# Performance work log

Measured on AMD Instinct MI355X. Metric: run time of the kernel, lower is better.

## Reference

```python
import jax, jax.numpy as jnp
import numpy as np

B, T, C, SIZE = 2, 4096, 1024, 1024
ROPE_DIM = 64
GAMMA = 0.96


def setup_inputs() -> dict:
    key = jax.random.key(0)
    ks = jax.random.split(key, 8)
    x = jax.random.normal(ks[0], (B, T, C), dtype=jnp.float32)
    group_mask = jax.random.randint(ks[1], (B, T), 0, 2).astype(jnp.float32)
    att_mask = jnp.ones((B, T), dtype=jnp.float32)
    # torch init: randn(in, out) / in
    W_Q = jax.random.normal(ks[2], (C, SIZE), dtype=jnp.float32) / C
    W_K = jax.random.normal(ks[3], (C, SIZE), dtype=jnp.float32) / C
    W_V = jax.random.normal(ks[4], (C, SIZE), dtype=jnp.float32) / C
    fc_w = jax.random.normal(ks[5], (SIZE, SIZE), dtype=jnp.float32) / np.float32(np.sqrt(SIZE))
    fc_b = jnp.zeros((SIZE,), dtype=jnp.float32)
    return dict(x=x, group_mask=group_mask, att_mask=att_mask,
                W_Q=W_Q, W_K=W_K, W_V=W_V, fc_w=fc_w, fc_b=fc_b)


def _rope(t, offset):
    # lucidrains rotate_queries_or_keys: rotate first ROPE_DIM features of
    # the last dim, interleaved-pair rotation, positions along axis -2.
    seq = t.shape[-2]
    inv = 1.0 / (10000.0 ** (jnp.arange(0, ROPE_DIM, 2, dtype=jnp.float32) / ROPE_DIM))
    pos = jnp.arange(seq, dtype=jnp.float32) + offset
    freqs = pos[:, None] * inv[None, :]              # [T, D/2]
    freqs = jnp.repeat(freqs, 2, axis=-1)            # [T, D]
    cos, sin = jnp.cos(freqs), jnp.sin(freqs)
    t_rot, t_pass = t[..., :ROPE_DIM], t[..., ROPE_DIM:]
    x1, x2 = t_rot[..., 0::2], t_rot[..., 1::2]
    rot_half = jnp.stack([-x2, x1], axis=-1).reshape(t_rot.shape)
    t_rot = t_rot * cos + rot_half * sin
    return jnp.concatenate([t_rot, t_pass], axis=-1)


def reference(x, group_mask, att_mask, W_Q, W_K, W_V, fc_w, fc_b):
    Bx, Tx, _ = x.shape
    # _qkv with apply_rope=True, apply_act=True (ReLU)
    Q = jax.nn.relu(_rope(x @ W_Q, 0))               # [B,T,SIZE]
    K = jax.nn.relu(_rope(x @ W_K, 0))
    V = jax.nn.relu(x @ W_V)
    n = jnp.arange(Tx)[:, None]
    m = jnp.arange(Tx)[None, :]
    causal = (n >= m)
    # decay mask D[n,m] = gamma^(n-m) for n>=m else 0
    D = jnp.where(causal, jnp.float32(GAMMA) ** (n - m).astype(jnp.float32), 0.0)
    # group mask G[b,n,m] = group_mask[b, n-m] for n>=m else 0
    idx = jnp.clip(n - m, 0, Tx - 1)                 # [T,T]
    G = group_mask[:, idx] * causal.astype(x.dtype)  # [B,T,T]
    A = jnp.einsum('bnd,bmd->bnm', Q, K)
    A = A * att_mask[:, :, None]                     # attention mask
    A = A * D[None, :, :]                            # decay mask
    A = A * G                                        # group mask
    y = jnp.einsum('bnm,bmd->bnd', A, V)
    y = y @ fc_w + fc_b
    return y
```

## Files before the change

### kernel.cpp

```cpp
#include <hip/hip_runtime.h>
#include <stdint.h>

typedef __attribute__((ext_vector_type(4))) float f32x4;
typedef __attribute__((ext_vector_type(8))) __bf16 bf16x8;
typedef __attribute__((ext_vector_type(4))) unsigned short u16x4;
typedef __attribute__((ext_vector_type(8))) unsigned short u16x8;

#define DEV __device__ __forceinline__

DEV unsigned short f2bf(float f) {
  union { float f; unsigned int u; } v; v.f = f;
  unsigned int r = v.u + 0x7fffu + ((v.u >> 16) & 1u);
  return (unsigned short)(r >> 16);
}

DEV void gl_lds16(const void* g, void* l) {
  __builtin_amdgcn_global_load_lds(
      (const __attribute__((address_space(1))) unsigned int*)g,
      (__attribute__((address_space(3))) unsigned int*)l, 16, 0, 0);
}


__global__ void prep_tabs(const float* __restrict__ gm,
                          float* __restrict__ costab, float* __restrict__ sintab,
                          float* __restrict__ wtab) {
  int idx = blockIdx.x * 256 + threadIdx.x;
  int n = idx >> 6, c = idx & 63, j = c >> 1;
  float inv = powf(10000.0f, -(float)(2 * j) / 64.0f);
  float ang = (float)n * inv;
  costab[idx] = cosf(ang);
  sintab[idx] = sinf(ang);
  if (idx < 1024) {
    int b = idx >> 9, d = idx & 511;
    wtab[idx] = gm[b * 4096 + d] * powf(0.96f, (float)d);
  }
}

__global__ void cvt_x(const float* __restrict__ x, unsigned short* __restrict__ xb) {
  size_t i8 = ((size_t)blockIdx.x * 256 + threadIdx.x) * 8;
  float4 a = *(const float4*)(x + i8);
  float4 b = *(const float4*)(x + i8 + 4);
  u16x8 o;
  o[0] = f2bf(a.x); o[1] = f2bf(a.y); o[2] = f2bf(a.z); o[3] = f2bf(a.w);
  o[4] = f2bf(b.x); o[5] = f2bf(b.y); o[6] = f2bf(b.z); o[7] = f2bf(b.w);
  *(u16x8*)(xb + i8) = o;
}

__global__ void transpose_cvt4(const float* __restrict__ s0, const float* __restrict__ s1,
                               const float* __restrict__ s2, const float* __restrict__ s3,
                               unsigned short* __restrict__ d0, unsigned short* __restrict__ d3) {
  __shared__ float tile[32][33];
  int z = blockIdx.z;
  const float* src = (z == 0) ? s0 : (z == 1) ? s1 : (z == 2) ? s2 : s3;
  unsigned short* dst = (z == 3) ? d3 : d0 + (size_t)z * 1024 * 1024;
  int tx = threadIdx.x & 31, ty = threadIdx.x >> 5;
  int c0 = blockIdx.x * 32, r0 = blockIdx.y * 32;
  #pragma unroll
  for (int j = 0; j < 4; j++)
    tile[ty + 8 * j][tx] = src[(size_t)(r0 + ty + 8 * j) * 1024 + c0 + tx];
  __syncthreads();
  #pragma unroll
  for (int j = 0; j < 4; j++)
    dst[(size_t)(c0 + ty + 8 * j) * 1024 + r0 + tx] = f2bf(tile[tx][ty + 8 * j]);
}

template<int EPI>
__global__ void __launch_bounds__(256, 4)
gemm128(const unsigned short* __restrict__ A,
        const unsigned short* __restrict__ Bt,
        unsigned short* __restrict__ q_out,
        unsigned short* __restrict__ k_out,
        unsigned short* __restrict__ vt_out,
        const float* __restrict__ costab,
        const float* __restrict__ sintab,
        float* __restrict__ f_out,
        const float* __restrict__ bias)
{
  constexpr int K = 1024;
  __shared__ char smem[32768];
  char* a_sm = smem;
  char* b_sm = smem + 16384;
  const int tid = threadIdx.x;
  const int lane = tid & 63;
  const int w = tid >> 6;
  const int wm = w >> 1, wn = w & 1;
  const int bm = blockIdx.x, bn = blockIdx.y;

  const f32x4 fz = {0.f, 0.f, 0.f, 0.f};
  f32x4 acc[4][4];
  #pragma unroll
  for (int i = 0; i < 4; i++)
    #pragma unroll
    for (int j = 0; j < 4; j++) acc[i][j] = fz;

  const unsigned short* Abase = A + (size_t)bm * 128 * K;
  const unsigned short* Bbase = Bt + (size_t)bn * 128 * K;

  for (int k0 = 0; k0 < K; k0 += 64) {
    __syncthreads();
    #pragma unroll
    for (int i = 0; i < 4; i++) {
      int tg = i * 256 + tid;
      int row = tg >> 3;
      int sl = (tg & 7) ^ (row & 7);
      gl_lds16(Abase + (size_t)row * K + k0 + sl * 8, a_sm + tg * 16);
    }
    #pragma unroll
    for (int i = 0; i < 4; i++) {
      int tg = i * 256 + tid;
      int row = tg >> 3;
      int sl = (tg & 7) ^ (row & 7);
      gl_lds16(Bbase + (size_t)row * K + k0 + sl * 8, b_sm + tg * 16);
    }
    __syncthreads();
    #pragma unroll
    for (int ks = 0; ks < 2; ks++) {
      int kb = ks * 64 + ((lane >> 4) << 4);
      bf16x8 af[4], bfv[4];
      #pragma unroll
      for (int f = 0; f < 4; f++) {
        int ar = wm * 64 + f * 16 + (lane & 15);
        af[f] = *(const bf16x8*)(a_sm + ar * 128 + (kb ^ ((ar & 7) << 4)));
        int br = wn * 64 + f * 16 + (lane & 15);
        bfv[f] = *(const bf16x8*)(b_sm + br * 128 + (kb ^ ((br & 7) << 4)));
      }
      #pragma unroll
      for (int fm = 0; fm < 4; fm++)
        #pragma unroll
        for (int fn = 0; fn < 4; fn++)
          acc[fm][fn] = __builtin_amdgcn_mfma_f32_16x16x32_bf16(af[fm], bfv[fn], acc[fm][fn], 0, 0, 0);
    }
  }

  const int rbase = bm * 128 + wm * 64 + ((lane >> 4) << 2);
  const int cbase = bn * 128 + wn * 64;

  if constexpr (EPI == 0) {
    #pragma unroll
    for (int fn = 0; fn < 4; fn++) {
      int col = cbase + fn * 16 + (lane & 15);
      int which = col >> 10;
      int c = col & 1023;
      #pragma unroll
      for (int fm = 0; fm < 4; fm++) {
        int row0 = rbase + fm * 16;
        float vals[4];
        #pragma unroll
        for (int r = 0; r < 4; r++) vals[r] = acc[fm][fn][r];
        if (which < 2) {
          if (c < 64) {
            #pragma unroll
            for (int r = 0; r < 4; r++) {
              float p = __shfl_xor(vals[r], 1);
              int n = (row0 + r) & 4095;
              float cs = costab[n * 64 + c];
              float sn = sintab[n * 64 + c];
              float rh = (c & 1) ? p : -p;
              vals[r] = vals[r] * cs + rh * sn;
            }
          }
          unsigned short* dst = (which == 0) ? q_out : k_out;
          #pragma unroll
          for (int r = 0; r < 4; r++) {
            float v = vals[r] > 0.f ? vals[r] : 0.f;
            dst[(size_t)(row0 + r) * 1024 + c] = f2bf(v);
          }
        } else {
          u16x4 sv;
          #pragma unroll
          for (int r = 0; r < 4; r++) {
            float v = vals[r] > 0.f ? vals[r] : 0.f;
            sv[r] = f2bf(v);
          }
          *(u16x4*)(vt_out + (size_t)c * 8192 + row0) = sv;
        }
      }
    }
  } else {
    #pragma unroll
    for (int fn = 0; fn < 4; fn++) {
      int col = cbase + fn * 16 + (lane & 15);
      float bv = bias[col];
      #pragma unroll
      for (int fm = 0; fm < 4; fm++) {
        int row0 = rbase + fm * 16;
        #pragma unroll
        for (int r = 0; r < 4; r++)
          f_out[(size_t)(row0 + r) * 1024 + col] = acc[fm][fn][r] + bv;
      }
    }
  }
}

__global__ void __launch_bounds__(512, 2)
attn_kernel(const unsigned short* __restrict__ Qb,
            const unsigned short* __restrict__ Kb,
            const unsigned short* __restrict__ Vt,
            const float* __restrict__ wtab,
            const float* __restrict__ att_mask,
            unsigned short* __restrict__ Yb)
{
  __shared__ alignas(16) unsigned char p_sm[32 * 640];
  __shared__ float wl[512];

  const int tid = threadIdx.x;
  const int lane = tid & 63;
  const int w = tid >> 6;

  const int id = blockIdx.x + blockIdx.y * 128;
  const int nid = (id & 7) * 32 + (id >> 3);
  const int qb = nid & 127;
  const int b = nid >> 7;

  const int q0 = qb * 32;
  const int base = b * 4096;
  const int kv0 = q0 - 256;

  if (tid < 512) wl[tid] = wtab[b * 512 + tid];

  const int wq = w >> 2, wk = w & 3;
  const int l15 = lane & 15, lhi = lane >> 4;

  const unsigned short* qptr =
      Qb + (size_t)(base + q0 + wq * 16 + l15) * 1024 + lhi * 8;
  const unsigned short* krow[5];
  #pragma unroll
  for (int f = 0; f < 5; f++) {
    int m = kv0 + wk * 80 + f * 16 + l15;
    m = m < 0 ? 0 : (m > 4095 ? 4095 : m);
    krow[f] = Kb + (size_t)(base + m) * 1024 + lhi * 8;
  }

  const f32x4 fz = {0.f, 0.f, 0.f, 0.f};
  f32x4 sacc[5];
  #pragma unroll
  for (int f = 0; f < 5; f++) sacc[f] = fz;

  for (int kk = 0; kk < 32; ++kk) {
    bf16x8 af = *(const bf16x8*)(qptr + kk * 32);
    #pragma unroll
    for (int f = 0; f < 5; f++) {
      bf16x8 bfv = *(const bf16x8*)(krow[f] + kk * 32);
      sacc[f] = __builtin_amdgcn_mfma_f32_16x16x32_bf16(af, bfv, sacc[f], 0, 0, 0);
    }
  }

  __syncthreads();

  #pragma unroll
  for (int f = 0; f < 5; f++) {
    int jj = wk * 80 + f * 16 + l15;
    int m = kv0 + jj;
    #pragma unroll
    for (int r = 0; r < 4; r++) {
      int i = wq * 16 + lhi * 4 + r;
      int d = 256 + i - jj;
      float wgt = (d >= 0 && m >= 0) ? wl[d] : 0.f;
      *(unsigned short*)(p_sm + i * 640 + ((jj * 2) ^ ((i & 7) << 4))) =
          f2bf(sacc[f][r] * wgt);
    }
  }
  __syncthreads();

  f32x4 yacc[2][8];
  #pragma unroll
  for (int i = 0; i < 2; i++)
    #pragma unroll
    for (int j = 0; j < 8; j++) yacc[i][j] = fz;

  const bool fastv = (kv0 >= 0) && (kv0 <= 3776);
  const unsigned short* vptr[8];
  #pragma unroll
  for (int f = 0; f < 8; f++) {
    int col = w * 128 + f * 16 + l15;
    vptr[f] = Vt + (size_t)col * 8192 + base + kv0 + lhi * 8;
  }

  for (int kt = 0; kt < 10; ++kt) {
    bf16x8 pa[2], vb[8];
    #pragma unroll
    for (int fm = 0; fm < 2; fm++) {
      int row = fm * 16 + l15;
      int cp = kt * 64 + lhi * 16;
      pa[fm] = *(const bf16x8*)(p_sm + row * 640 + (cp ^ ((row & 7) << 4)));
    }
    if (fastv) {
      #pragma unroll
      for (int f = 0; f < 8; f++) vb[f] = *(const bf16x8*)(vptr[f] + kt * 32);
    } else {
      int m = kv0 + kt * 32 + lhi * 8;
      m = m < 0 ? 0 : (m > 4088 ? 4088 : m);
      #pragma unroll
      for (int f = 0; f < 8; f++) {
        int col = w * 128 + f * 16 + l15;
        vb[f] = *(const bf16x8*)(Vt + (size_t)col * 8192 + base + m);
      }
    }
    #pragma unroll
    for (int fm = 0; fm < 2; fm++)
      #pragma unroll
      for (int fn = 0; fn < 8; fn++)
        yacc[fm][fn] = __builtin_amdgcn_mfma_f32_16x16x32_bf16(pa[fm], vb[fn], yacc[fm][fn], 0, 0, 0);
  }

  #pragma unroll
  for (int fm = 0; fm < 2; fm++) {
    #pragma unroll
    for (int r = 0; r < 4; r++) {
      int n = q0 + fm * 16 + lhi * 4 + r;
      float am = att_mask[base + n];
      #pragma unroll
      for (int fn = 0; fn < 8; fn++) {
        int col = w * 128 + fn * 16 + l15;
        Yb[(size_t)(base + n) * 1024 + col] = f2bf(yacc[fm][fn][r] * am);
      }
    }
  }
}

extern "C" void kernel_launch(void* const* d_in, const int* in_sizes, int n_in,
                              void* d_out, int out_size, void* d_ws, size_t ws_size,
                              hipStream_t stream)
{
  (void)in_sizes; (void)n_in; (void)out_size;
  const float* x   = (const float*)d_in[0];
  const float* gm  = (const float*)d_in[1];
  const float* am  = (const float*)d_in[2];
  const float* wq  = (const float*)d_in[3];
  const float* wk  = (const float*)d_in[4];
  const float* wv  = (const float*)d_in[5];
  const float* fcw = (const float*)d_in[6];
  const float* fcb = (const float*)d_in[7];
  float* out = (float*)d_out;

  char* p = (char*)d_ws;
  unsigned short* xb    = (unsigned short*)p; p += (size_t)8192 * 1024 * 2;
  unsigned short* Qb    = (unsigned short*)p; p += (size_t)8192 * 1024 * 2;
  unsigned short* Kb    = (unsigned short*)p; p += (size_t)8192 * 1024 * 2;
  unsigned short* Vt    = (unsigned short*)p; p += (size_t)8192 * 1024 * 2;
  unsigned short* Ybuf  = (unsigned short*)p; p += (size_t)8192 * 1024 * 2;
  unsigned short* WqkvT = (unsigned short*)p; p += (size_t)3072 * 1024 * 2;
  unsigned short* FcwT  = (unsigned short*)p; p += (size_t)1024 * 1024 * 2;
  float* costab = (float*)p; p += (size_t)4096 * 64 * 4;
  float* sintab = (float*)p; p += (size_t)4096 * 64 * 4;
  float* wtab   = (float*)p; p += 4096;
  if ((size_t)(p - (char*)d_ws) > ws_size) return;

  prep_tabs<<<1024, 256, 0, stream>>>(gm, costab, sintab, wtab);
  cvt_x<<<4096, 256, 0, stream>>>(x, xb);
  transpose_cvt4<<<dim3(32, 32, 4), 256, 0, stream>>>(wq, wk, wv, fcw, WqkvT, FcwT);

  gemm128<0><<<dim3(64, 24), 256, 0, stream>>>(xb, WqkvT, Qb, Kb, Vt, costab, sintab, nullptr, nullptr);
  attn_kernel<<<dim3(128, 2), 512, 0, stream>>>(Qb, Kb, Vt, wtab, am, Ybuf);
  gemm128<1><<<dim3(64, 8), 256, 0, stream>>>(Ybuf, FcwT, nullptr, nullptr, nullptr, nullptr, nullptr, out, fcb);
}
```

Before: 259.1 us.

## Replace QKV GEMM with 256x256 tile, 8-wave, LDS double-buffered pipelined kernel

```diff
diff --git a/kernel.cpp b/kernel.cpp
--- a/kernel.cpp
+++ b/kernel.cpp
@@ -19,6 +19,11 @@
       (const __attribute__((address_space(1))) unsigned int*)g,
       (__attribute__((address_space(3))) unsigned int*)l, 16, 0, 0);
 }
+
+#define SBAR() __builtin_amdgcn_s_barrier()
+#define LGKM0() asm volatile("s_waitcnt lgkmcnt(0)" ::: "memory")
+#define VMC6() asm volatile("s_waitcnt vmcnt(6)" ::: "memory")
+#define VMC0() asm volatile("s_waitcnt vmcnt(0)" ::: "memory")
 
 
 __global__ void prep_tabs(const float* __restrict__ gm,
@@ -64,17 +69,195 @@
     dst[(size_t)(c0 + ty + 8 * j) * 1024 + r0 + tx] = f2bf(tile[tx][ty + 8 * j]);
 }
 
-template<int EPI>
-__global__ void __launch_bounds__(256, 4)
-gemm128(const unsigned short* __restrict__ A,
-        const unsigned short* __restrict__ Bt,
-        unsigned short* __restrict__ q_out,
-        unsigned short* __restrict__ k_out,
-        unsigned short* __restrict__ vt_out,
-        const float* __restrict__ costab,
-        const float* __restrict__ sintab,
-        float* __restrict__ f_out,
-        const float* __restrict__ bias)
+
+DEV void stage_half(const unsigned short* __restrict__ g0, int kcol, char* regn, int tid) {
+  #pragma unroll
+  for (int i = 0; i < 2; i++) {
+    int tg = i * 512 + tid;
+    int row = tg >> 3;
+    int ch = tg & 7;
+    gl_lds16(g0 + (size_t)row * 1024 + kcol + ((ch ^ (row & 7)) << 3), regn + tg * 16);
+  }
+}
+
+DEV void read_a4(bf16x8 (&af)[4][2], const char* regn, int wm, int lane) {
+  #pragma unroll
+  for (int f = 0; f < 4; f++) {
+    int row = wm * 64 + f * 16 + (lane & 15);
+    #pragma unroll
+    for (int ks = 0; ks < 2; ks++) {
+      int c = ks * 4 + (lane >> 4);
+      af[f][ks] = *(const bf16x8*)(regn + row * 128 + ((c ^ (row & 7)) << 4));
+    }
+  }
+}
+
+DEV void read_b2(bf16x8 (&bfr)[2][2], const char* regn, int wn, int lane) {
+  #pragma unroll
+  for (int g = 0; g < 2; g++) {
+    int row = wn * 32 + g * 16 + (lane & 15);
+    #pragma unroll
+    for (int ks = 0; ks < 2; ks++) {
+      int c = ks * 4 + (lane >> 4);
+      bfr[g][ks] = *(const bf16x8*)(regn + row * 128 + ((c ^ (row & 7)) << 4));
+    }
+  }
+}
+
+template<int MB, int NB>
+DEV void mfma16(f32x4 (&acc)[8][4], const bf16x8 (&af)[4][2], const bf16x8 (&bfr)[2][2]) {
+  #pragma unroll
+  for (int ks = 0; ks < 2; ks++)
+    #pragma unroll
+    for (int f = 0; f < 4; f++)
+      #pragma unroll
+      for (int g = 0; g < 2; g++)
+        acc[MB + f][NB + g] =
+            __builtin_amdgcn_mfma_f32_16x16x32_bf16(af[f][ks], bfr[g][ks], acc[MB + f][NB + g], 0, 0, 0);
+}
+
+__global__ void __launch_bounds__(512, 2)
+gemm256_qkv(const unsigned short* __restrict__ A,
+            const unsigned short* __restrict__ Bt,
+            unsigned short* __restrict__ q_out,
+            unsigned short* __restrict__ k_out,
+            unsigned short* __restrict__ vt_out,
+            const float* __restrict__ costab,
+            const float* __restrict__ sintab)
+{
+  extern __shared__ char smem[];
+  constexpr int NT = 16;
+  const int tid = threadIdx.x;
+  const int lane = tid & 63;
+  const int w = tid >> 6;
+  const int wm = w >> 2, wn = w & 3;
+  const int bm = blockIdx.x, bn = blockIdx.y;
+
+  char* const a0_0 = smem;
+  char* const a1_0 = smem + 16384;
+  char* const b0_0 = smem + 32768;
+  char* const b1_0 = smem + 49152;
+  char* const a0_1 = smem + 65536;
+  char* const a1_1 = smem + 81920;
+  char* const b0_1 = smem + 98304;
+  char* const b1_1 = smem + 114688;
+
+  const unsigned short* Ab = A + (size_t)bm * 256 * 1024;
+  const unsigned short* Bb = Bt + (size_t)bn * 256 * 1024;
+  const unsigned short* A0g = Ab;
+  const unsigned short* A1g = Ab + (size_t)128 * 1024;
+  const unsigned short* B0g = Bb;
+  const unsigned short* B1g = Bb + (size_t)128 * 1024;
+
+  const f32x4 fz = {0.f, 0.f, 0.f, 0.f};
+  f32x4 acc[8][4];
+  #pragma unroll
+  for (int i = 0; i < 8; i++)
+    #pragma unroll
+    for (int j = 0; j < 4; j++) acc[i][j] = fz;
+
+  stage_half(A0g, 0, a0_0, tid);
+  stage_half(B0g, 0, b0_0, tid);
+  stage_half(B1g, 0, b1_0, tid);
+  stage_half(A1g, 0, a1_0, tid);
+  stage_half(A0g, 64, a0_1, tid);
+  stage_half(B1g, 64, b1_1, tid);
+  stage_half(A1g, 64, a1_1, tid);
+  VMC6();
+  SBAR();
+
+#define TILE_BODY(cA0, cA1, cB0, cB1, nB0, T)                                   \
+  {                                                                             \
+    bf16x8 af[4][2], bfr[2][2];                                                 \
+                                                              \
+    read_a4(af, cA0, wm, lane);                                                 \
+    read_b2(bfr, cB0, wn, lane);                                                \
+    if ((T) + 1 < NT) stage_half(B0g, ((T) + 1) * 64, nB0, tid);                \
+    SBAR(); LGKM0();                                                            \
+    __builtin_amdgcn_s_setprio(1);                                              \
+    mfma16<0, 0>(acc, af, bfr);                                                 \
+    __builtin_amdgcn_s_setprio(0);                                              \
+    SBAR();                                                                     \
+                                               \
+    read_b2(bfr, cB1, wn, lane);                                                \
+    if ((T) + 2 < NT) stage_half(A0g, ((T) + 2) * 64, cA0, tid);                \
+    SBAR(); LGKM0();                                                            \
+    __builtin_amdgcn_s_setprio(1);                                              \
+    mfma16<0, 2>(acc, af, bfr);                                                 \
+    __builtin_amdgcn_s_setprio(0);                                              \
+    SBAR();                                                                     \
+                                               \
+    read_a4(af, cA1, wm, lane);                                                 \
+    if ((T) + 2 < NT) stage_half(B1g, ((T) + 2) * 64, cB1, tid);                \
+    SBAR(); LGKM0();                                                            \
+    __builtin_amdgcn_s_setprio(1);                                              \
+    mfma16<4, 2>(acc, af, bfr);                                                 \
+    __builtin_amdgcn_s_setprio(0);                                              \
+    SBAR();                                                                     \
+                               \
+    read_b2(bfr, cB0, wn, lane);                                                \
+    if ((T) + 2 < NT) stage_half(A1g, ((T) + 2) * 64, cA1, tid);                \
+    SBAR(); LGKM0();                                                            \
+    __builtin_amdgcn_s_setprio(1);                                              \
+    mfma16<4, 0>(acc, af, bfr);                                                 \
+    __builtin_amdgcn_s_setprio(0);                                              \
+    if ((T) < NT - 2) { VMC6(); } else { VMC0(); }                              \
+    SBAR();                                                                     \
+  }
+
+  for (int tp = 0; tp < NT / 2; ++tp) {
+    TILE_BODY(a0_0, a1_0, b0_0, b1_0, b0_1, 2 * tp);
+    TILE_BODY(a0_1, a1_1, b0_1, b1_1, b0_0, 2 * tp + 1);
+  }
+#undef TILE_BODY
+
+  #pragma unroll
+  for (int n = 0; n < 4; n++) {
+    int col = bn * 256 + (n >> 1) * 128 + wn * 32 + (n & 1) * 16 + (lane & 15);
+    int which = col >> 10;
+    int c = col & 1023;
+    #pragma unroll
+    for (int m = 0; m < 8; m++) {
+      int row0 = bm * 256 + (m >> 2) * 128 + wm * 64 + (m & 3) * 16 + ((lane >> 4) << 2);
+      float vals[4];
+      #pragma unroll
+      for (int r = 0; r < 4; r++) vals[r] = acc[m][n][r];
+      if (which < 2) {
+        if (c < 64) {
+          #pragma unroll
+          for (int r = 0; r < 4; r++) {
+            float p = __shfl_xor(vals[r], 1);
+            int nn = (row0 + r) & 4095;
+            float cs = costab[nn * 64 + c];
+            float sn = sintab[nn * 64 + c];
+            float rh = (c & 1) ? p : -p;
+            vals[r] = vals[r] * cs + rh * sn;
+          }
+        }
+        unsigned short* dst = (which == 0) ? q_out : k_out;
+        #pragma unroll
+        for (int r = 0; r < 4; r++) {
+          float v = vals[r] > 0.f ? vals[r] : 0.f;
+          dst[(size_t)(row0 + r) * 1024 + c] = f2bf(v);
+        }
+      } else {
+        u16x4 sv;
+        #pragma unroll
+        for (int r = 0; r < 4; r++) {
+          float v = vals[r] > 0.f ? vals[r] : 0.f;
+          sv[r] = f2bf(v);
+        }
+        *(u16x4*)(vt_out + (size_t)c * 8192 + row0) = sv;
+      }
+    }
+  }
+}
+
+__global__ void __launch_bounds__(256, 2)
+gemm128_fc(const unsigned short* __restrict__ A,
+           const unsigned short* __restrict__ Bt,
+           float* __restrict__ f_out,
+           const float* __restrict__ bias)
 {
   constexpr int K = 1024;
   __shared__ char smem[32768];
@@ -134,60 +317,16 @@
 
   const int rbase = bm * 128 + wm * 64 + ((lane >> 4) << 2);
   const int cbase = bn * 128 + wn * 64;
-
-  if constexpr (EPI == 0) {
-    #pragma unroll
-    for (int fn = 0; fn < 4; fn++) {
-      int col = cbase + fn * 16 + (lane & 15);
-      int which = col >> 10;
-      int c = col & 1023;
-      #pragma unroll
-      for (int fm = 0; fm < 4; fm++) {
-        int row0 = rbase + fm * 16;
-        float vals[4];
-        #pragma unroll
-        for (int r = 0; r < 4; r++) vals[r] = acc[fm][fn][r];
-        if (which < 2) {
-          if (c < 64) {
-            #pragma unroll
-            for (int r = 0; r < 4; r++) {
-              float p = __shfl_xor(vals[r], 1);
-              int n = (row0 + r) & 4095;
-              float cs = costab[n * 64 + c];
-              float sn = sintab[n * 64 + c];
-              float rh = (c & 1) ? p : -p;
-              vals[r] = vals[r] * cs + rh * sn;
-            }
-          }
-          unsigned short* dst = (which == 0) ? q_out : k_out;
-          #pragma unroll
-          for (int r = 0; r < 4; r++) {
-            float v = vals[r] > 0.f ? vals[r] : 0.f;
-            dst[(size_t)(row0 + r) * 1024 + c] = f2bf(v);
-          }
-        } else {
-          u16x4 sv;
-          #pragma unroll
-          for (int r = 0; r < 4; r++) {
-            float v = vals[r] > 0.f ? vals[r] : 0.f;
-            sv[r] = f2bf(v);
-          }
-          *(u16x4*)(vt_out + (size_t)c * 8192 + row0) = sv;
-        }
-      }
-    }
-  } else {
-    #pragma unroll
-    for (int fn = 0; fn < 4; fn++) {
-      int col = cbase + fn * 16 + (lane & 15);
-      float bv = bias[col];
-      #pragma unroll
-      for (int fm = 0; fm < 4; fm++) {
-        int row0 = rbase + fm * 16;
-        #pragma unroll
-        for (int r = 0; r < 4; r++)
-          f_out[(size_t)(row0 + r) * 1024 + col] = acc[fm][fn][r] + bv;
-      }
+  #pragma unroll
+  for (int fn = 0; fn < 4; fn++) {
+    int col = cbase + fn * 16 + (lane & 15);
+    float bv = bias[col];
+    #pragma unroll
+    for (int fm = 0; fm < 4; fm++) {
+      int row0 = rbase + fm * 16;
+      #pragma unroll
+      for (int r = 0; r < 4; r++)
+        f_out[(size_t)(row0 + r) * 1024 + col] = acc[fm][fn][r] + bv;
     }
   }
 }
@@ -346,11 +485,14 @@
   float* wtab   = (float*)p; p += 4096;
   if ((size_t)(p - (char*)d_ws) > ws_size) return;
 
+  hipFuncSetAttribute((const void*)gemm256_qkv,
+                      hipFuncAttributeMaxDynamicSharedMemorySize, 131072);
+
   prep_tabs<<<1024, 256, 0, stream>>>(gm, costab, sintab, wtab);
   cvt_x<<<4096, 256, 0, stream>>>(x, xb);
   transpose_cvt4<<<dim3(32, 32, 4), 256, 0, stream>>>(wq, wk, wv, fcw, WqkvT, FcwT);
 
-  gemm128<0><<<dim3(64, 24), 256, 0, stream>>>(xb, WqkvT, Qb, Kb, Vt, costab, sintab, nullptr, nullptr);
+  gemm256_qkv<<<dim3(32, 12), 512, 131072, stream>>>(xb, WqkvT, Qb, Kb, Vt, costab, sintab);
   attn_kernel<<<dim3(128, 2), 512, 0, stream>>>(Qb, Kb, Vt, wtab, am, Ybuf);
-  gemm128<1><<<dim3(64, 8), 256, 0, stream>>>(Ybuf, FcwT, nullptr, nullptr, nullptr, nullptr, nullptr, out, fcb);
-}
+  gemm128_fc<<<dim3(64, 8), 256, 0, stream>>>(Ybuf, FcwT, out, fcb);
+}
```

After: 257.1 us. About the same (-0.8%).
